# Kernel optimization log

Hardware: AMD Instinct MI355X
Metric: run time of the kernel (lower is better)

## Reference

```python
import jax, jax.numpy as jnp
import numpy as np

N_NODES = 100000


def _gcn_conv(x, edge_index, W, b):
    """PyG GCNConv: add self-loops, symmetric deg^-1/2 normalization, scatter-add."""
    N = x.shape[0]
    h = x @ W  # [N, out]
    src = edge_index[0]
    dst = edge_index[1]
    loop = jnp.arange(N, dtype=src.dtype)
    src = jnp.concatenate([src, loop])
    dst = jnp.concatenate([dst, loop])
    deg = jax.ops.segment_sum(jnp.ones(src.shape[0], dtype=h.dtype), dst, num_segments=N)
    dinv = jnp.where(deg > 0, jax.lax.rsqrt(deg), 0.0)
    norm = dinv[src] * dinv[dst]  # [E+N]
    msgs = h[src] * norm[:, None]  # gather + scale
    out = jax.ops.segment_sum(msgs, dst, num_segments=N)  # scatter-add
    return out + b


def setup_inputs() -> dict:
    key = jax.random.key(0)
    k1, k2, k3, k4 = jax.random.split(key, 4)
    F_IN, H = 512, 16
    x = jax.random.normal(k1, (N_NODES, F_IN), dtype=jnp.float32)
    edge_index = jax.random.randint(k2, (2, 3200000), 0, N_NODES, dtype=jnp.int64)
    # Glorot init like PyG GCNConv
    lim = np.sqrt(6.0 / (F_IN + H)).astype(np.float32)
    W1 = jax.random.uniform(k3, (F_IN, H), dtype=jnp.float32, minval=-lim, maxval=lim)
    b1 = jnp.zeros((H,), dtype=jnp.float32)
    return {"x": x, "edge_index": edge_index, "W1": W1, "b1": b1}


def reference(x, edge_index, W1, b1):
    # forward: relu(GCNConv(x)); dropout is identity in eval; log_softmax over features
    h = jax.nn.relu(_gcn_conv(x, edge_index, W1, b1))
    return jax.nn.log_softmax(h, axis=1)
```

## Files before the change

kernel.cpp:

```cpp
#include <hip/hip_runtime.h>
#include <hip/hip_bf16.h>
#include <stdint.h>

#define N_NODES 100000
#define F_IN    512
#define HOUT    16

#define BSH   8
#define NBUK  391
#define CAP   9216
#define CHUNK 4096
#define GEMM_BLOCKS 782

typedef __attribute__((ext_vector_type(8))) short bf16x8;
typedef __attribute__((ext_vector_type(4))) float f32x4;

__device__ __forceinline__ short f2bf(float f) {
    union { float f; uint32_t u; } v; v.f = f;
    uint32_t r = (v.u + 0x7FFFu + ((v.u >> 16) & 1u)) >> 16;
    return (short)r;
}
__device__ __forceinline__ float bf2f(uint32_t bits16) {
    union { uint32_t u; float f; } v; v.u = bits16 << 16;
    return v.f;
}

__device__ __forceinline__ int edge_at(const void* ei, int64_t idx, uint32_t is64) {
    if (is64) return (int)((const long long*)ei)[idx];
    return ((const int*)ei)[idx];
}

__global__ void k_init(const uint32_t* __restrict__ e_u32, uint32_t* __restrict__ flag,
                       uint32_t* __restrict__ bucket_woff) {
    const int t = threadIdx.x;
    if (t < NBUK) bucket_woff[t] = 0u;
    if (t == 0) {
        uint32_t o = 0;
        #pragma unroll
        for (int i = 1; i < 32; i += 2) o |= e_u32[i];
        flag[0] = (o == 0u) ? 1u : 0u;
    }
}

__global__ __launch_bounds__(512, 4) void k_fused(const void* __restrict__ ei, int E, int nchunks,
                                                  const uint32_t* __restrict__ flag,
                                                  uint32_t* __restrict__ bucket_woff,
                                                  uint32_t* __restrict__ gpairs,
                                                  const float* __restrict__ x,
                                                  const float* __restrict__ W,
                                                  ushort* __restrict__ hb) {
    __shared__ uint32_t h[512];
    __shared__ uint32_t ex[512];
    __shared__ uint32_t pcnt[512];
    __shared__ uint32_t gbase[512];
    __shared__ __align__(16) uint32_t big[CHUNK + CHUNK / 2];

    const int t = threadIdx.x;

    if ((int)blockIdx.x < nchunks) {
        uint32_t* sorted = big;
        uint16_t* sbuck  = (uint16_t*)(big + CHUNK);
        const uint32_t is64 = flag[0];
        const int base = blockIdx.x * CHUNK;
        const int chunk_n = min(CHUNK, E - base);
        const bool evenE = ((E & 1) == 0);

        h[t] = 0;
        __syncthreads();

        uint32_t pr[8];
        uint16_t bk[8];
        #pragma unroll
        for (int k = 0; k < 4; ++k) {
            const int e0 = base + k * 1024 + 2 * t;
            uint32_t s0 = 0, s1 = 0, d0 = 0, d1 = 0;
            const bool ok0 = (e0 < E), ok1 = (e0 + 1 < E);
            if (ok1 && evenE) {
                if (is64) {
                    ulonglong2 S = *(const ulonglong2*)((const long long*)ei + e0);
                    ulonglong2 D = *(const ulonglong2*)((const long long*)ei + (int64_t)E + e0);
                    s0 = (uint32_t)S.x; s1 = (uint32_t)S.y;
                    d0 = (uint32_t)D.x; d1 = (uint32_t)D.y;
                } else {
                    uint2 S = *(const uint2*)((const int*)ei + e0);
                    uint2 D = *(const uint2*)((const int*)ei + (int64_t)E + e0);
                    s0 = S.x; s1 = S.y; d0 = D.x; d1 = D.y;
                }
            } else {
                if (ok0) { s0 = (uint32_t)edge_at(ei, e0, is64);
                           d0 = (uint32_t)edge_at(ei, (int64_t)E + e0, is64); }
                if (ok1) { s1 = (uint32_t)edge_at(ei, e0 + 1, is64);
                           d1 = (uint32_t)edge_at(ei, (int64_t)E + e0 + 1, is64); }
            }
            bk[2*k]   = 0xFFFFu;
            bk[2*k+1] = 0xFFFFu;
            if (ok0) {
                uint32_t b = d0 >> BSH;
                pr[2*k] = (s0 << BSH) | (d0 & 255u);
                bk[2*k] = (uint16_t)b;
                atomicAdd(&h[b], 1u);
            }
            if (ok1) {
                uint32_t b = d1 >> BSH;
                pr[2*k+1] = (s1 << BSH) | (d1 & 255u);
                bk[2*k+1] = (uint16_t)b;
                atomicAdd(&h[b], 1u);
            }
        }
        __syncthreads();

        const uint32_t hv = h[t];
        uint32_t v = hv;
        #pragma unroll
        for (int d = 1; d < 64; d <<= 1) {
            uint32_t u = __shfl_up(v, d, 64);
            if ((t & 63) >= d) v += u;
        }
        h[t] = v;
        __syncthreads();
        uint32_t wbase = 0;
        const int w = t >> 6;
        for (int w2 = 0; w2 < w; ++w2) wbase += h[w2 * 64 + 63];
        const uint32_t exv = wbase + v - hv;
        ex[t] = exv;
        pcnt[t] = exv;
        if (t < NBUK) gbase[t] = atomicAdd(&bucket_woff[t], hv);
        __syncthreads();

        #pragma unroll
        for (int k = 0; k < 8; ++k) {
            if (bk[k] != 0xFFFFu) {
                uint32_t slot = atomicAdd(&pcnt[bk[k]], 1u);
                sorted[slot] = pr[k];
                sbuck[slot] = bk[k];
            }
        }
        __syncthreads();

        #pragma unroll
        for (int k = 0; k < 8; ++k) {
            int i = k * 512 + t;
            if (i < chunk_n) {
                uint32_t b = sbuck[i];
                uint32_t pos = gbase[b] + ((uint32_t)i - ex[b]);
                gpairs[(size_t)b * CAP + pos] = sorted[i];
            }
        }
    } else {
        ushort* wlds = (ushort*)big;
        #pragma unroll
        for (int r = 0; r < 2; ++r) {
            const int ent = t + 512 * r;
            const int s  = ent >> 6;
            const int hf = (ent >> 4) & 3;
            const int c  = ent & 15;
            ushort u[8];
            #pragma unroll
            for (int e = 0; e < 8; ++e)
                u[e] = (ushort)f2bf(W[(32 * s + 8 * hf + e) * HOUT + c]);
            *(ulonglong2*)(wlds + (size_t)ent * 8) = *(const ulonglong2*)u;
        }
        __syncthreads();

        const int lane = t & 63;
        const int wid  = t >> 6;
        const int tile = ((int)blockIdx.x - nchunks) * 8 + wid;
        if (tile * 16 >= N_NODES) return;
        const int c    = lane & 15;
        const int half = lane >> 4;

        const int row = tile * 16 + c;
        const float* xr = x + (int64_t)row * F_IN + half * 8;
        const ushort* wb = wlds + (size_t)(half * 16 + c) * 8;

        float4 xa[3], xb[3];
        #pragma unroll
        for (int p = 0; p < 3; ++p) {
            xa[p] = *(const float4*)(xr + 32 * p);
            xb[p] = *(const float4*)(xr + 32 * p + 4);
        }

        f32x4 acc = {0.f, 0.f, 0.f, 0.f};
        #pragma unroll
        for (int s = 0; s < 16; ++s) {
            const int p = s % 3;
            bf16x8 bf = *(const bf16x8*)(wb + (size_t)s * 512);
            bf16x8 af;
            af[0] = f2bf(xa[p].x); af[1] = f2bf(xa[p].y);
            af[2] = f2bf(xa[p].z); af[3] = f2bf(xa[p].w);
            af[4] = f2bf(xb[p].x); af[5] = f2bf(xb[p].y);
            af[6] = f2bf(xb[p].z); af[7] = f2bf(xb[p].w);
            if (s + 3 < 16) {
                xa[p] = *(const float4*)(xr + 32 * (s + 3));
                xb[p] = *(const float4*)(xr + 32 * (s + 3) + 4);
            }
            acc = __builtin_amdgcn_mfma_f32_16x16x32_bf16(af, bf, acc, 0, 0, 0);
        }

        #pragma unroll
        for (int r = 0; r < 4; ++r) {
            int orow = tile * 16 + 4 * half + r;
            hb[(int64_t)orow * HOUT + c] = (ushort)f2bf(acc[r]);
        }
    }
}

__global__ __launch_bounds__(256) void k_hist(const uint32_t* __restrict__ bucket_woff,
                                              const uint32_t* __restrict__ gpairs,
                                              uint32_t* __restrict__ cnt,
                                              ushort* __restrict__ hb) {
    const int b = blockIdx.x;
    const int t = threadIdx.x;
    const uint32_t count = bucket_woff[b];
    const uint32_t* gp = gpairs + (size_t)b * CAP;

    __shared__ uint32_t lc[256];
    lc[t] = 0;
    __syncthreads();
    for (uint32_t i = t; i < count; i += 256)
        atomicAdd(&lc[gp[i] & 255u], 1u);
    __syncthreads();

    const int gn = (b << BSH) + t;
    if (gn < N_NODES) {
        const uint32_t deg = lc[t];
        cnt[gn] = deg;
        const float dinv = rsqrtf((float)(deg + 1u));
        ushort* row = hb + (size_t)gn * HOUT;
        ulonglong4 rv = *(const ulonglong4*)row;
        ushort u[16];
        *(ulonglong4*)u = rv;
        #pragma unroll
        for (int q = 0; q < 16; ++q)
            u[q] = (ushort)f2bf(bf2f(u[q]) * dinv);
        *(ulonglong4*)row = *(const ulonglong4*)u;
    }
}

__global__ __launch_bounds__(1024) void k_sortagg(const uint32_t* __restrict__ bucket_woff,
                                                  const uint32_t* __restrict__ gpairs,
                                                  const uint32_t* __restrict__ cnt,
                                                  const ushort* __restrict__ hb,
                                                  const float* __restrict__ bias,
                                                  float* __restrict__ out) {
    const int bk = blockIdx.x;
    const int t = threadIdx.x;
    const uint32_t count = bucket_woff[bk];
    const uint32_t* gp = gpairs + (size_t)bk * CAP;
    const uint32_t* hb32 = (const uint32_t*)hb;

    __shared__ uint32_t lc[256];
    __shared__ uint32_t st[256];
    __shared__ uint32_t cur[256];
    __shared__ uint32_t lsrc[CAP];

    if (t < 256) {
        int gn = (bk << BSH) + t;
        lc[t] = (gn < N_NODES) ? cnt[gn] : 0u;
    }
    __syncthreads();
    if (t < 256) {
        const uint32_t hv = lc[t];
        uint32_t v = hv;
        #pragma unroll
        for (int d = 1; d < 64; d <<= 1) {
            uint32_t u = __shfl_up(v, d, 64);
            if ((t & 63) >= d) v += u;
        }
        cur[t] = v;
    }
    __syncthreads();
    if (t < 256) {
        uint32_t wb = 0;
        const int w = t >> 6;
        for (int w2 = 0; w2 < w; ++w2) wb += cur[w2 * 64 + 63];
        st[t] = wb + cur[t] - lc[t];
    }
    __syncthreads();
    if (t < 256) cur[t] = st[t];
    __syncthreads();

    for (uint32_t i = t; i < count; i += 1024) {
        uint32_t p = gp[i];
        uint32_t pos = atomicAdd(&cur[p & 255u], 1u);
        lsrc[pos] = p >> BSH;
    }
    __syncthreads();

    const int f8 = t & 7;
    const int g  = t >> 3;
    const float b0 = bias[2 * f8];
    const float b1 = bias[2 * f8 + 1];

    #pragma unroll
    for (int i = 0; i < 2; ++i) {
        int dl = g + 128 * i;
        int gn = (bk << BSH) + dl;
        if (gn >= N_NODES) break;
        const uint32_t s0 = st[dl];
        const uint32_t n  = lc[dl];

        float a0 = 0.f, a1 = 0.f;
        uint32_t j = 0;
        for (; j + 4 <= n; j += 4) {
            uint32_t sA = lsrc[s0 + j],     sB = lsrc[s0 + j + 1];
            uint32_t sC = lsrc[s0 + j + 2], sD = lsrc[s0 + j + 3];
            uint32_t uA = hb32[(size_t)sA * 8 + f8];
            uint32_t uB = hb32[(size_t)sB * 8 + f8];
            uint32_t uC = hb32[(size_t)sC * 8 + f8];
            uint32_t uD = hb32[(size_t)sD * 8 + f8];
            a0 += (bf2f(uA & 0xFFFFu) + bf2f(uB & 0xFFFFu))
                + (bf2f(uC & 0xFFFFu) + bf2f(uD & 0xFFFFu));
            a1 += (bf2f(uA >> 16) + bf2f(uB >> 16))
                + (bf2f(uC >> 16) + bf2f(uD >> 16));
        }
        for (; j < n; ++j) {
            uint32_t u = hb32[(size_t)lsrc[s0 + j] * 8 + f8];
            a0 += bf2f(u & 0xFFFFu);
            a1 += bf2f(u >> 16);
        }

        const float dinv = rsqrtf((float)(n + 1u));
        const uint32_t us = hb32[(size_t)gn * 8 + f8];
        float v0 = fmaxf(fmaf(dinv, a0 + bf2f(us & 0xFFFFu), b0), 0.f);
        float v1 = fmaxf(fmaf(dinv, a1 + bf2f(us >> 16), b1), 0.f);

        float m = fmaxf(v0, v1);
        #pragma unroll
        for (int d = 1; d < 8; d <<= 1) m = fmaxf(m, __shfl_xor(m, d, 8));
        float sum = __expf(v0 - m) + __expf(v1 - m);
        #pragma unroll
        for (int d = 1; d < 8; d <<= 1) sum += __shfl_xor(sum, d, 8);
        const float ls = m + __logf(sum);

        float2 o; o.x = v0 - ls; o.y = v1 - ls;
        ((float2*)out)[(size_t)gn * 8 + f8] = o;
    }
}

extern "C" void kernel_launch(void* const* d_in, const int* in_sizes, int n_in,
                              void* d_out, int out_size, void* d_ws, size_t ws_size,
                              hipStream_t stream) {
    const float* x  = (const float*)d_in[0];
    const void*  ei = d_in[1];
    const float* W  = (const float*)d_in[2];
    const float* b  = (const float*)d_in[3];
    float* out = (float*)d_out;
    const int E = in_sizes[1] / 2;
    const int nchunks = (E + CHUNK - 1) / CHUNK;

    char* ws = (char*)d_ws;
    uint32_t* flag        = (uint32_t*)ws;
    uint32_t* bucket_woff = (uint32_t*)(ws + 1024);
    uint32_t* gpairs      = (uint32_t*)(ws + (1 << 20));
    ushort*   hb          = (ushort*)(ws + (16 << 20));
    uint32_t* cnt         = (uint32_t*)(ws + (20 << 20));

    k_init<<<1, 512, 0, stream>>>((const uint32_t*)ei, flag, bucket_woff);
    k_fused<<<nchunks + GEMM_BLOCKS, 512, 0, stream>>>(ei, E, nchunks, flag,
                                                       bucket_woff, gpairs, x, W, hb);
    k_hist<<<NBUK, 256, 0, stream>>>(bucket_woff, gpairs, cnt, hb);
    k_sortagg<<<NBUK, 1024, 0, stream>>>(bucket_woff, gpairs, cnt, hb, b, out);
}
```

Baseline: 107.2 us.

## Merge all stages into one persistent cooperative kernel with grid syncs

Replaces the four separate launches (init, fused bucket/GEMM, histogram, sort-aggregate) with one persistent cooperative kernel of 256 blocks of 1024 threads. Stages are separated by grid-wide syncs, and the flag init moves to a memset plus a per-block flag check. This removes launch overhead and inter-kernel gaps. In exchange, the bucketing and GEMM phases no longer overlap, parallelism is capped at 256 blocks, and the per-bucket phases now leave many blocks idle (391 buckets over 256 blocks).

```diff
diff --git a/kernel.cpp b/kernel.cpp
--- a/kernel.cpp
+++ b/kernel.cpp
@@ -1,6 +1,9 @@
 #include <hip/hip_runtime.h>
+#include <hip/hip_cooperative_groups.h>
 #include <hip/hip_bf16.h>
 #include <stdint.h>
+
+namespace cg = cooperative_groups;
 
 #define N_NODES 100000
 #define F_IN    512
@@ -10,7 +13,8 @@
 #define NBUK  391
 #define CAP   9216
 #define CHUNK 4096
-#define GEMM_BLOCKS 782
+#define NTILES 6250
+#define GRIDN 256
 
 typedef __attribute__((ext_vector_type(8))) short bf16x8;
 typedef __attribute__((ext_vector_type(4))) float f32x4;
@@ -30,49 +34,44 @@
     return ((const int*)ei)[idx];
 }
 
-__global__ void k_init(const uint32_t* __restrict__ e_u32, uint32_t* __restrict__ flag,
-                       uint32_t* __restrict__ bucket_woff) {
+__global__ __launch_bounds__(1024, 4) void k_mega(
+        const void* __restrict__ ei, int E, int nchunks,
+        uint32_t* __restrict__ woff, uint32_t* __restrict__ gpairs,
+        const float* __restrict__ x, const float* __restrict__ W,
+        ushort* __restrict__ hb, uint32_t* __restrict__ cnt,
+        const float* __restrict__ bias, float* __restrict__ out) {
+    __shared__ __align__(16) uint32_t pool[10240];
+    __shared__ uint32_t sh_flag;
     const int t = threadIdx.x;
-    if (t < NBUK) bucket_woff[t] = 0u;
+
     if (t == 0) {
         uint32_t o = 0;
         #pragma unroll
-        for (int i = 1; i < 32; i += 2) o |= e_u32[i];
-        flag[0] = (o == 0u) ? 1u : 0u;
-    }
-}
-
-__global__ __launch_bounds__(512, 4) void k_fused(const void* __restrict__ ei, int E, int nchunks,
-                                                  const uint32_t* __restrict__ flag,
-                                                  uint32_t* __restrict__ bucket_woff,
-                                                  uint32_t* __restrict__ gpairs,
-                                                  const float* __restrict__ x,
-                                                  const float* __restrict__ W,
-                                                  ushort* __restrict__ hb) {
-    __shared__ uint32_t h[512];
-    __shared__ uint32_t ex[512];
-    __shared__ uint32_t pcnt[512];
-    __shared__ uint32_t gbase[512];
-    __shared__ __align__(16) uint32_t big[CHUNK + CHUNK / 2];
-
-    const int t = threadIdx.x;
-
-    if ((int)blockIdx.x < nchunks) {
-        uint32_t* sorted = big;
-        uint16_t* sbuck  = (uint16_t*)(big + CHUNK);
-        const uint32_t is64 = flag[0];
-        const int base = blockIdx.x * CHUNK;
+        for (int i = 1; i < 32; i += 2) o |= ((const uint32_t*)ei)[i];
+        sh_flag = (o == 0u) ? 1u : 0u;
+    }
+    __syncthreads();
+    const uint32_t is64 = sh_flag;
+    const bool evenE = ((E & 1) == 0);
+
+    uint32_t* h      = pool;
+    uint32_t* ex     = pool + 512;
+    uint32_t* pcnt   = pool + 1024;
+    uint32_t* gbase  = pool + 1536;
+    uint32_t* sorted = pool + 2048;
+    uint16_t* sbuck  = (uint16_t*)(pool + 6144);
+
+    for (int c = blockIdx.x; c < nchunks; c += GRIDN) {
+        if (t < 512) h[t] = 0;
+        __syncthreads();
+        const int base = c * CHUNK;
         const int chunk_n = min(CHUNK, E - base);
-        const bool evenE = ((E & 1) == 0);
-
-        h[t] = 0;
-        __syncthreads();
-
-        uint32_t pr[8];
-        uint16_t bk[8];
-        #pragma unroll
-        for (int k = 0; k < 4; ++k) {
-            const int e0 = base + k * 1024 + 2 * t;
+
+        uint32_t pr[4];
+        uint16_t bk[4];
+        #pragma unroll
+        for (int k = 0; k < 2; ++k) {
+            const int e0 = base + k * 2048 + 2 * t;
             uint32_t s0 = 0, s1 = 0, d0 = 0, d1 = 0;
             const bool ok0 = (e0 < E), ok1 = (e0 + 1 < E);
             if (ok1 && evenE) {
@@ -109,26 +108,30 @@
         }
         __syncthreads();
 
-        const uint32_t hv = h[t];
-        uint32_t v = hv;
-        #pragma unroll
-        for (int d = 1; d < 64; d <<= 1) {
-            uint32_t u = __shfl_up(v, d, 64);
-            if ((t & 63) >= d) v += u;
-        }
-        h[t] = v;
-        __syncthreads();
-        uint32_t wbase = 0;
-        const int w = t >> 6;
-        for (int w2 = 0; w2 < w; ++w2) wbase += h[w2 * 64 + 63];
-        const uint32_t exv = wbase + v - hv;
-        ex[t] = exv;
-        pcnt[t] = exv;
-        if (t < NBUK) gbase[t] = atomicAdd(&bucket_woff[t], hv);
-        __syncthreads();
-
-        #pragma unroll
-        for (int k = 0; k < 8; ++k) {
+        uint32_t hv = 0, v = 0;
+        if (t < 512) {
+            hv = h[t]; v = hv;
+            #pragma unroll
+            for (int d = 1; d < 64; d <<= 1) {
+                uint32_t u = __shfl_up(v, d, 64);
+                if ((t & 63) >= d) v += u;
+            }
+            h[t] = v;
+        }
+        __syncthreads();
+        if (t < 512) {
+            uint32_t wbase = 0;
+            const int w = t >> 6;
+            for (int w2 = 0; w2 < w; ++w2) wbase += h[w2 * 64 + 63];
+            const uint32_t exv = wbase + v - hv;
+            ex[t] = exv;
+            pcnt[t] = exv;
+            if (t < NBUK) gbase[t] = atomicAdd(&woff[t], hv);
+        }
+        __syncthreads();
+
+        #pragma unroll
+        for (int k = 0; k < 4; ++k) {
             if (bk[k] != 0xFFFFu) {
                 uint32_t slot = atomicAdd(&pcnt[bk[k]], 1u);
                 sorted[slot] = pr[k];
@@ -138,203 +141,193 @@
         __syncthreads();
 
         #pragma unroll
-        for (int k = 0; k < 8; ++k) {
-            int i = k * 512 + t;
+        for (int k = 0; k < 4; ++k) {
+            int i = k * 1024 + t;
             if (i < chunk_n) {
                 uint32_t b = sbuck[i];
                 uint32_t pos = gbase[b] + ((uint32_t)i - ex[b]);
                 gpairs[(size_t)b * CAP + pos] = sorted[i];
             }
         }
-    } else {
-        ushort* wlds = (ushort*)big;
-        #pragma unroll
-        for (int r = 0; r < 2; ++r) {
-            const int ent = t + 512 * r;
-            const int s  = ent >> 6;
-            const int hf = (ent >> 4) & 3;
-            const int c  = ent & 15;
-            ushort u[8];
-            #pragma unroll
-            for (int e = 0; e < 8; ++e)
-                u[e] = (ushort)f2bf(W[(32 * s + 8 * hf + e) * HOUT + c]);
-            *(ulonglong2*)(wlds + (size_t)ent * 8) = *(const ulonglong2*)u;
-        }
-        __syncthreads();
-
+        __syncthreads();
+    }
+
+    __syncthreads();
+    ushort* wlds = (ushort*)(pool + 2048);
+    {
+        const int ent = t;
+        const int s  = ent >> 6;
+        const int hf = (ent >> 4) & 3;
+        const int c2 = ent & 15;
+        ushort u[8];
+        #pragma unroll
+        for (int e = 0; e < 8; ++e)
+            u[e] = (ushort)f2bf(W[(32 * s + 8 * hf + e) * HOUT + c2]);
+        *(ulonglong2*)(wlds + (size_t)ent * 8) = *(const ulonglong2*)u;
+    }
+    __syncthreads();
+
+    {
         const int lane = t & 63;
         const int wid  = t >> 6;
-        const int tile = ((int)blockIdx.x - nchunks) * 8 + wid;
-        if (tile * 16 >= N_NODES) return;
-        const int c    = lane & 15;
+        const int c2   = lane & 15;
         const int half = lane >> 4;
-
-        const int row = tile * 16 + c;
-        const float* xr = x + (int64_t)row * F_IN + half * 8;
-        const ushort* wb = wlds + (size_t)(half * 16 + c) * 8;
-
-        float4 xa[3], xb[3];
-        #pragma unroll
-        for (int p = 0; p < 3; ++p) {
-            xa[p] = *(const float4*)(xr + 32 * p);
-            xb[p] = *(const float4*)(xr + 32 * p + 4);
-        }
-
-        f32x4 acc = {0.f, 0.f, 0.f, 0.f};
-        #pragma unroll
-        for (int s = 0; s < 16; ++s) {
-            const int p = s % 3;
-            bf16x8 bf = *(const bf16x8*)(wb + (size_t)s * 512);
-            bf16x8 af;
-            af[0] = f2bf(xa[p].x); af[1] = f2bf(xa[p].y);
-            af[2] = f2bf(xa[p].z); af[3] = f2bf(xa[p].w);
-            af[4] = f2bf(xb[p].x); af[5] = f2bf(xb[p].y);
-            af[6] = f2bf(xb[p].z); af[7] = f2bf(xb[p].w);
-            if (s + 3 < 16) {
-                xa[p] = *(const float4*)(xr + 32 * (s + 3));
-                xb[p] = *(const float4*)(xr + 32 * (s + 3) + 4);
-            }
-            acc = __builtin_amdgcn_mfma_f32_16x16x32_bf16(af, bf, acc, 0, 0, 0);
-        }
-
-        #pragma unroll
-        for (int r = 0; r < 4; ++r) {
-            int orow = tile * 16 + 4 * half + r;
-            hb[(int64_t)orow * HOUT + c] = (ushort)f2bf(acc[r]);
-        }
-    }
-}
-
-__global__ __launch_bounds__(256) void k_hist(const uint32_t* __restrict__ bucket_woff,
-                                              const uint32_t* __restrict__ gpairs,
-                                              uint32_t* __restrict__ cnt,
-                                              ushort* __restrict__ hb) {
-    const int b = blockIdx.x;
-    const int t = threadIdx.x;
-    const uint32_t count = bucket_woff[b];
-    const uint32_t* gp = gpairs + (size_t)b * CAP;
-
-    __shared__ uint32_t lc[256];
-    lc[t] = 0;
-    __syncthreads();
-    for (uint32_t i = t; i < count; i += 256)
-        atomicAdd(&lc[gp[i] & 255u], 1u);
-    __syncthreads();
-
-    const int gn = (b << BSH) + t;
-    if (gn < N_NODES) {
-        const uint32_t deg = lc[t];
-        cnt[gn] = deg;
-        const float dinv = rsqrtf((float)(deg + 1u));
-        ushort* row = hb + (size_t)gn * HOUT;
-        ulonglong4 rv = *(const ulonglong4*)row;
-        ushort u[16];
-        *(ulonglong4*)u = rv;
-        #pragma unroll
-        for (int q = 0; q < 16; ++q)
-            u[q] = (ushort)f2bf(bf2f(u[q]) * dinv);
-        *(ulonglong4*)row = *(const ulonglong4*)u;
-    }
-}
-
-__global__ __launch_bounds__(1024) void k_sortagg(const uint32_t* __restrict__ bucket_woff,
-                                                  const uint32_t* __restrict__ gpairs,
-                                                  const uint32_t* __restrict__ cnt,
-                                                  const ushort* __restrict__ hb,
-                                                  const float* __restrict__ bias,
-                                                  float* __restrict__ out) {
-    const int bk = blockIdx.x;
-    const int t = threadIdx.x;
-    const uint32_t count = bucket_woff[bk];
-    const uint32_t* gp = gpairs + (size_t)bk * CAP;
+        const ushort* wb = wlds + (size_t)(half * 16 + c2) * 8;
+
+        for (int tile = blockIdx.x * 16 + wid; tile < NTILES; tile += GRIDN * 16) {
+            const int row = tile * 16 + c2;
+            const float* xr = x + (int64_t)row * F_IN + half * 8;
+
+            float4 xa[3], xb2[3];
+            #pragma unroll
+            for (int p = 0; p < 3; ++p) {
+                xa[p]  = *(const float4*)(xr + 32 * p);
+                xb2[p] = *(const float4*)(xr + 32 * p + 4);
+            }
+            f32x4 acc = {0.f, 0.f, 0.f, 0.f};
+            #pragma unroll
+            for (int s = 0; s < 16; ++s) {
+                const int p = s % 3;
+                bf16x8 bf = *(const bf16x8*)(wb + (size_t)s * 512);
+                bf16x8 af;
+                af[0] = f2bf(xa[p].x);  af[1] = f2bf(xa[p].y);
+                af[2] = f2bf(xa[p].z);  af[3] = f2bf(xa[p].w);
+                af[4] = f2bf(xb2[p].x); af[5] = f2bf(xb2[p].y);
+                af[6] = f2bf(xb2[p].z); af[7] = f2bf(xb2[p].w);
+                if (s + 3 < 16) {
+                    xa[p]  = *(const float4*)(xr + 32 * (s + 3));
+                    xb2[p] = *(const float4*)(xr + 32 * (s + 3) + 4);
+                }
+                acc = __builtin_amdgcn_mfma_f32_16x16x32_bf16(af, bf, acc, 0, 0, 0);
+            }
+            #pragma unroll
+            for (int r = 0; r < 4; ++r) {
+                int orow = tile * 16 + 4 * half + r;
+                hb[(int64_t)orow * HOUT + c2] = (ushort)f2bf(acc[r]);
+            }
+        }
+    }
+
+    cg::this_grid().sync();
+
+    uint32_t* lc = pool;
+    for (int b = blockIdx.x; b < NBUK; b += GRIDN) {
+        __syncthreads();
+        if (t < 256) lc[t] = 0;
+        __syncthreads();
+        const uint32_t count = woff[b];
+        const uint32_t* gp = gpairs + (size_t)b * CAP;
+        for (uint32_t i = t; i < count; i += 1024)
+            atomicAdd(&lc[gp[i] & 255u], 1u);
+        __syncthreads();
+        const int gn = (b << BSH) + t;
+        if (t < 256 && gn < N_NODES) {
+            const uint32_t deg = lc[t];
+            cnt[gn] = deg;
+            const float dinv = rsqrtf((float)(deg + 1u));
+            ushort* row = hb + (size_t)gn * HOUT;
+            ulonglong4 rv = *(const ulonglong4*)row;
+            ushort u[16];
+            *(ulonglong4*)u = rv;
+            #pragma unroll
+            for (int q = 0; q < 16; ++q)
+                u[q] = (ushort)f2bf(bf2f(u[q]) * dinv);
+            *(ulonglong4*)row = *(const ulonglong4*)u;
+        }
+    }
+
+    cg::this_grid().sync();
+
+    uint32_t* st   = pool + 256;
+    uint32_t* cur  = pool + 512;
+    uint32_t* lsrc = pool + 768;
     const uint32_t* hb32 = (const uint32_t*)hb;
-
-    __shared__ uint32_t lc[256];
-    __shared__ uint32_t st[256];
-    __shared__ uint32_t cur[256];
-    __shared__ uint32_t lsrc[CAP];
-
-    if (t < 256) {
-        int gn = (bk << BSH) + t;
-        lc[t] = (gn < N_NODES) ? cnt[gn] : 0u;
-    }
-    __syncthreads();
-    if (t < 256) {
-        const uint32_t hv = lc[t];
-        uint32_t v = hv;
-        #pragma unroll
-        for (int d = 1; d < 64; d <<= 1) {
-            uint32_t u = __shfl_up(v, d, 64);
-            if ((t & 63) >= d) v += u;
-        }
-        cur[t] = v;
-    }
-    __syncthreads();
-    if (t < 256) {
-        uint32_t wb = 0;
-        const int w = t >> 6;
-        for (int w2 = 0; w2 < w; ++w2) wb += cur[w2 * 64 + 63];
-        st[t] = wb + cur[t] - lc[t];
-    }
-    __syncthreads();
-    if (t < 256) cur[t] = st[t];
-    __syncthreads();
-
-    for (uint32_t i = t; i < count; i += 1024) {
-        uint32_t p = gp[i];
-        uint32_t pos = atomicAdd(&cur[p & 255u], 1u);
-        lsrc[pos] = p >> BSH;
-    }
-    __syncthreads();
-
     const int f8 = t & 7;
     const int g  = t >> 3;
     const float b0 = bias[2 * f8];
     const float b1 = bias[2 * f8 + 1];
 
-    #pragma unroll
-    for (int i = 0; i < 2; ++i) {
-        int dl = g + 128 * i;
-        int gn = (bk << BSH) + dl;
-        if (gn >= N_NODES) break;
-        const uint32_t s0 = st[dl];
-        const uint32_t n  = lc[dl];
-
-        float a0 = 0.f, a1 = 0.f;
-        uint32_t j = 0;
-        for (; j + 4 <= n; j += 4) {
-            uint32_t sA = lsrc[s0 + j],     sB = lsrc[s0 + j + 1];
-            uint32_t sC = lsrc[s0 + j + 2], sD = lsrc[s0 + j + 3];
-            uint32_t uA = hb32[(size_t)sA * 8 + f8];
-            uint32_t uB = hb32[(size_t)sB * 8 + f8];
-            uint32_t uC = hb32[(size_t)sC * 8 + f8];
-            uint32_t uD = hb32[(size_t)sD * 8 + f8];
-            a0 += (bf2f(uA & 0xFFFFu) + bf2f(uB & 0xFFFFu))
-                + (bf2f(uC & 0xFFFFu) + bf2f(uD & 0xFFFFu));
-            a1 += (bf2f(uA >> 16) + bf2f(uB >> 16))
-                + (bf2f(uC >> 16) + bf2f(uD >> 16));
-        }
-        for (; j < n; ++j) {
-            uint32_t u = hb32[(size_t)lsrc[s0 + j] * 8 + f8];
-            a0 += bf2f(u & 0xFFFFu);
-            a1 += bf2f(u >> 16);
-        }
-
-        const float dinv = rsqrtf((float)(n + 1u));
-        const uint32_t us = hb32[(size_t)gn * 8 + f8];
-        float v0 = fmaxf(fmaf(dinv, a0 + bf2f(us & 0xFFFFu), b0), 0.f);
-        float v1 = fmaxf(fmaf(dinv, a1 + bf2f(us >> 16), b1), 0.f);
-
-        float m = fmaxf(v0, v1);
-        #pragma unroll
-        for (int d = 1; d < 8; d <<= 1) m = fmaxf(m, __shfl_xor(m, d, 8));
-        float sum = __expf(v0 - m) + __expf(v1 - m);
-        #pragma unroll
-        for (int d = 1; d < 8; d <<= 1) sum += __shfl_xor(sum, d, 8);
-        const float ls = m + __logf(sum);
-
-        float2 o; o.x = v0 - ls; o.y = v1 - ls;
-        ((float2*)out)[(size_t)gn * 8 + f8] = o;
+    for (int bk_ = blockIdx.x; bk_ < NBUK; bk_ += GRIDN) {
+        __syncthreads();
+        if (t < 256) {
+            int gn = (bk_ << BSH) + t;
+            lc[t] = (gn < N_NODES) ? cnt[gn] : 0u;
+        }
+        __syncthreads();
+        if (t < 256) {
+            const uint32_t hv = lc[t];
+            uint32_t v = hv;
+            #pragma unroll
+            for (int d = 1; d < 64; d <<= 1) {
+                uint32_t u = __shfl_up(v, d, 64);
+                if ((t & 63) >= d) v += u;
+            }
+            cur[t] = v;
+        }
+        __syncthreads();
+        if (t < 256) {
+            uint32_t wb2 = 0;
+            const int w = t >> 6;
+            for (int w2 = 0; w2 < w; ++w2) wb2 += cur[w2 * 64 + 63];
+            st[t] = wb2 + cur[t] - lc[t];
+        }
+        __syncthreads();
+        if (t < 256) cur[t] = st[t];
+        __syncthreads();
+
+        const uint32_t count = woff[bk_];
+        const uint32_t* gp = gpairs + (size_t)bk_ * CAP;
+        for (uint32_t i = t; i < count; i += 1024) {
+            uint32_t p = gp[i];
+            uint32_t pos = atomicAdd(&cur[p & 255u], 1u);
+            lsrc[pos] = p >> BSH;
+        }
+        __syncthreads();
+
+        #pragma unroll
+        for (int i2 = 0; i2 < 2; ++i2) {
+            int dl = g + 128 * i2;
+            int gn = (bk_ << BSH) + dl;
+            if (gn >= N_NODES) break;
+            const uint32_t s0 = st[dl];
+            const uint32_t n  = lc[dl];
+
+            float a0 = 0.f, a1 = 0.f;
+            uint32_t j = 0;
+            for (; j + 4 <= n; j += 4) {
+                uint32_t sA = lsrc[s0 + j],     sB = lsrc[s0 + j + 1];
+                uint32_t sC = lsrc[s0 + j + 2], sD = lsrc[s0 + j + 3];
+                uint32_t uA = hb32[(size_t)sA * 8 + f8];
+                uint32_t uB = hb32[(size_t)sB * 8 + f8];
+                uint32_t uC = hb32[(size_t)sC * 8 + f8];
+                uint32_t uD = hb32[(size_t)sD * 8 + f8];
+                a0 += (bf2f(uA & 0xFFFFu) + bf2f(uB & 0xFFFFu))
+                    + (bf2f(uC & 0xFFFFu) + bf2f(uD & 0xFFFFu));
+                a1 += (bf2f(uA >> 16) + bf2f(uB >> 16))
+                    + (bf2f(uC >> 16) + bf2f(uD >> 16));
+            }
+            for (; j < n; ++j) {
+                uint32_t u = hb32[(size_t)lsrc[s0 + j] * 8 + f8];
+                a0 += bf2f(u & 0xFFFFu);
+                a1 += bf2f(u >> 16);
+            }
+
+            const float dinv = rsqrtf((float)(n + 1u));
+            const uint32_t us = hb32[(size_t)gn * 8 + f8];
+            float v0 = fmaxf(fmaf(dinv, a0 + bf2f(us & 0xFFFFu), b0), 0.f);
+            float v1 = fmaxf(fmaf(dinv, a1 + bf2f(us >> 16), b1), 0.f);
+
+            float m = fmaxf(v0, v1);
+            #pragma unroll
+            for (int d = 1; d < 8; d <<= 1) m = fmaxf(m, __shfl_xor(m, d, 8));
+            float sum = __expf(v0 - m) + __expf(v1 - m);
+            #pragma unroll
+            for (int d = 1; d < 8; d <<= 1) sum += __shfl_xor(sum, d, 8);
+            const float ls = m + __logf(sum);
+
+            float2 o; o.x = v0 - ls; o.y = v1 - ls;
+            ((float2*)out)[(size_t)gn * 8 + f8] = o;
+        }
     }
 }
 
@@ -346,19 +339,24 @@
     const float* W  = (const float*)d_in[2];
     const float* b  = (const float*)d_in[3];
     float* out = (float*)d_out;
-    const int E = in_sizes[1] / 2;
-    const int nchunks = (E + CHUNK - 1) / CHUNK;
+    int E = in_sizes[1] / 2;
+    int nchunks = (E + CHUNK - 1) / CHUNK;
 
     char* ws = (char*)d_ws;
-    uint32_t* flag        = (uint32_t*)ws;
-    uint32_t* bucket_woff = (uint32_t*)(ws + 1024);
-    uint32_t* gpairs      = (uint32_t*)(ws + (1 << 20));
-    ushort*   hb          = (ushort*)(ws + (16 << 20));
-    uint32_t* cnt         = (uint32_t*)(ws + (20 << 20));
-
-    k_init<<<1, 512, 0, stream>>>((const uint32_t*)ei, flag, bucket_woff);
-    k_fused<<<nchunks + GEMM_BLOCKS, 512, 0, stream>>>(ei, E, nchunks, flag,
-                                                       bucket_woff, gpairs, x, W, hb);
-    k_hist<<<NBUK, 256, 0, stream>>>(bucket_woff, gpairs, cnt, hb);
-    k_sortagg<<<NBUK, 1024, 0, stream>>>(bucket_woff, gpairs, cnt, hb, b, out);
-}
+    uint32_t* woff   = (uint32_t*)(ws + 1024);
+    uint32_t* gpairs = (uint32_t*)(ws + (1 << 20));
+    ushort*   hb     = (ushort*)(ws + (16 << 20));
+    uint32_t* cnt    = (uint32_t*)(ws + (20 << 20));
+
+    hipMemsetAsync(woff, 0, NBUK * sizeof(uint32_t), stream);
+
+    void* args[] = {
+        (void*)&ei, (void*)&E, (void*)&nchunks,
+        (void*)&woff, (void*)&gpairs,
+        (void*)&x, (void*)&W,
+        (void*)&hb, (void*)&cnt,
+        (void*)&b, (void*)&out
+    };
+    hipLaunchCooperativeKernel((void*)k_mega, dim3(GRIDN), dim3(1024),
+                               args, 0, stream);
+}
```

New measurement: 178.6 us. 66.6% more time.
